# Kernel optimization log

Hardware: AMD Instinct MI355X
Metric: run time of the kernel (lower is better)

The kernel has to match this reference:

```python
import jax, jax.numpy as jnp
import numpy as np
from jax import lax

NEAR = 0.0
FAR = 2.4
NUM_STEPS = 16
NUM_REFINE = 8
LOG_THRESH = 0.0  # -log(1/0.5 - 1) for threshold=0.5
EPS = float(np.finfo(np.float32).eps)


def predict(points, feature, W1, b1, W2, b2, W3, b3):
    # points: [b, m, 3]; feature: [b, F] conditioning vector broadcast per point
    b, m, _ = points.shape
    feat = jnp.broadcast_to(feature[:, None, :], (b, m, feature.shape[-1]))
    x = jnp.concatenate([points, feat], axis=-1)
    h = jax.nn.relu(x @ W1 + b1)
    h = jax.nn.relu(h @ W2 + b2)
    return (h @ W3 + b3)[..., 0]  # [b, m] occupancy logits


def _safe_denom(dc):
    # torch.copysign(torch.max(torch.abs(dc), eps), dc)
    return jnp.copysign(jnp.maximum(jnp.abs(dc), EPS), dc)


def ray_march(ray0, ray_dirs, feature, params):
    b, n, _ = ray0.shape
    steps = jnp.linspace(0.0, 1.0, NUM_STEPS, dtype=ray0.dtype)
    dists = NEAR + steps * (FAR - NEAR)  # [S]
    # [b, n, S, 3]
    pts = ray0[:, :, None, :] + dists[None, None, :, None] * ray_dirs[:, :, None, :]
    f = predict(pts.reshape(b, n * NUM_STEPS, 3), feature, *params)
    f = f.reshape(b, n, NUM_STEPS) - LOG_THRESH
    # first outside->inside crossing per ray
    cross = (f[..., :-1] < 0) & (f[..., 1:] >= 0)  # [b, n, S-1]
    mask = jnp.any(cross, axis=-1)
    idx = jnp.argmax(cross, axis=-1)  # index of first crossing
    take = lambda a, i: jnp.take_along_axis(a, i[..., None], axis=-1)[..., 0]
    f_low = take(f, idx)
    f_high = take(f, idx + 1)
    d_low = dists[idx]
    d_high = dists[idx + 1]
    # secant refinement (fixed NUM_REFINE iterations, fully vectorized per ray)
    for _ in range(NUM_REFINE):
        d_new = d_low - f_low * (d_high - d_low) / _safe_denom(f_high - f_low)
        f_new = predict(ray0 + d_new[..., None] * ray_dirs, feature, *params) - LOG_THRESH
        below = f_new < 0
        d_low = jnp.where(below, d_new, d_low)
        f_low = jnp.where(below, f_new, f_low)
        d_high = jnp.where(below, d_high, d_new)
        f_high = jnp.where(below, f_new, f_high)
    d_pred = d_low - f_low * (d_high - d_low) / _safe_denom(f_high - f_low)
    d_pred = jnp.where(mask, d_pred, FAR)
    p_pred = ray0 + d_pred[..., None] * ray_dirs
    return d_pred, p_pred, mask


def setup_inputs() -> dict:
    key = jax.random.key(0)
    ks = jax.random.split(key, 6)
    B, N, F, H = 4, 16384, 32, 128
    ray0 = jax.random.normal(ks[0], (B, N, 3), jnp.float32) * 0.5
    rd = jax.random.normal(ks[1], (B, N, 3), jnp.float32)
    ray_dirs = rd / jnp.linalg.norm(rd, axis=-1, keepdims=True)
    feature = jax.random.normal(ks[2], (B, F), jnp.float32)
    W1 = jax.random.normal(ks[3], (3 + F, H), jnp.float32) / np.sqrt(3 + F)
    b1 = jnp.zeros((H,), jnp.float32)
    W2 = jax.random.normal(ks[4], (H, H), jnp.float32) / np.sqrt(H)
    b2 = jnp.zeros((H,), jnp.float32)
    W3 = jax.random.normal(ks[5], (H, 1), jnp.float32) / np.sqrt(H)
    b3 = jnp.zeros((1,), jnp.float32)
    return {"ray0": ray0, "ray_dirs": ray_dirs, "feature": feature,
            "W1": W1, "b1": b1, "W2": W2, "b2": b2, "W3": W3, "b3": b3}


def reference(ray0, ray_dirs, feature, W1, b1, W2, b2, W3, b3):
    params = (W1, b1, W2, b2, W3, b3)
    d_out, p_out, mask = ray_march(ray0, ray_dirs, feature, params)
    return d_out, p_out, mask
```

## Files before the change

### kernel.cpp

```cpp
#include <hip/hip_runtime.h>
#include <hip/hip_bf16.h>

typedef short short8 __attribute__((ext_vector_type(8)));
typedef float f32x4  __attribute__((ext_vector_type(4)));

static constexpr int   NPB  = 16384;
static constexpr int   NR   = 4 * NPB;
static constexpr int   NS   = 16;
static constexpr int   H    = 128;
static constexpr int   NPTS = NR * NS;
static constexpr int   NCHUNK2 = NR / 8;
static constexpr int   FIXCAP = 131072;
static constexpr float FARV = 2.4f;
static constexpr float EPSF = 1.1920928955078125e-07f;
static constexpr float FTHRESH = 0.03f;


__device__ __forceinline__ unsigned bf16hi(float x) {
    unsigned u = __float_as_uint(x);
    return (u + 0x7FFFu + ((u >> 16) & 1u)) >> 16;
}
__device__ __forceinline__ void split_bf16(float x, short& hi, short& lo) {
    unsigned h = bf16hi(x);
    float hf = __uint_as_float(h << 16);
    unsigned l = __float_as_uint(x - hf) >> 16;
    hi = (short)h; lo = (short)l;
}
__device__ __forceinline__ unsigned pk_bf16(float a, float b) {
    __hip_bfloat162 p = __float22bfloat162_rn(make_float2(a, b));
    unsigned u;
    __builtin_memcpy(&u, &p, sizeof(u));
    return u;
}

__global__ void k_setup(const float* __restrict__ W1, const float* __restrict__ b1,
                        const float* __restrict__ W2, const float* __restrict__ feat,
                        float* __restrict__ cva, short* __restrict__ w2f,
                        int* __restrict__ count, int* __restrict__ fixcnt)
{
    int t = blockIdx.x * blockDim.x + threadIdx.x;
    if (t == 0) { *count = 0; *fixcnt = 0; }
    if (t < 4 * H) {
        int b = t >> 7, kk = t & (H - 1);
        float acc = b1[kk];
#pragma unroll
        for (int i = 0; i < 32; ++i)
            acc = fmaf(feat[b * 32 + i], W1[(3 + i) * H + kk], acc);
        cva[b * H + kk] = acc;
    }
    {
        int lane = t & 63, ks = (t >> 6) & 3, part = (t >> 8) & 1;
        int nt = (t >> 9) & 1, w = (t >> 10) & 3;
        int n = w * 32 + nt * 16 + (lane & 15);
        int kb = ks * 32 + (lane >> 4) * 8;
        short8 v;
#pragma unroll
        for (int j = 0; j < 8; ++j) {
            short hi, lo;
            split_bf16(W2[(kb + j) * H + n], hi, lo);
            v[j] = part ? lo : hi;
        }
        ((short8*)w2f)[((w * 4 + nt * 2 + part) * 4 + ks) * 64 + lane] = v;
    }
}

__global__ __launch_bounds__(256, 2) void k_marchx(
    const float* __restrict__ ray0, const float* __restrict__ dirs,
    const float* __restrict__ W1,   const float* __restrict__ cva,
    const float* __restrict__ b2,   const float* __restrict__ W3,
    const float* __restrict__ b3p,  const short* __restrict__ w2f,
    float* __restrict__ f_all, int* __restrict__ fixlist, int* __restrict__ fixcnt)
{
    __shared__ __align__(16) short hAhi[16384];
    __shared__ float fpart[2][4][128];
    const int tid = threadIdx.x;
    const int w = tid >> 6, lane = tid & 63;
    const int q = lane >> 4, ln15 = lane & 15;

    const short8* wf8 = (const short8*)w2f;
    short8 Bh0[4], Bl0[4], Bh1[4], Bl1[4];
#pragma unroll
    for (int ks = 0; ks < 4; ++ks) {
        Bh0[ks] = wf8[((w * 4 + 0) * 4 + ks) * 64 + lane];
        Bl0[ks] = wf8[((w * 4 + 1) * 4 + ks) * 64 + lane];
        Bh1[ks] = wf8[((w * 4 + 2) * 4 + ks) * 64 + lane];
        Bl1[ks] = wf8[((w * 4 + 3) * 4 + ks) * 64 + lane];
    }
    const int nb0 = w * 32 + q * 4;
    float b2a[4], b2b[4], w3a[4], w3b[4];
#pragma unroll
    for (int reg = 0; reg < 4; ++reg) {
        b2a[reg] = b2[nb0 + reg];       b2b[reg] = b2[nb0 + 16 + reg];
        w3a[reg] = W3[nb0 + reg];       w3b[reg] = W3[nb0 + 16 + reg];
    }
    const float b3v  = *b3p;

    const int rr = tid & 7;
    const int kt = tid >> 3;
    const int qp = (tid >> 4) & 3;
    const int j0 = ((tid >> 3) & 1) * 4;
    short* hwp = hAhi + ((w * 64 + rr + 16 * qp) * 8 + j0);
    const float4 wxv = ((const float4*)W1)[kt];
    const float4 wyv = ((const float4*)(W1 + H))[kt];
    const float4 wzv = ((const float4*)(W1 + 2 * H))[kt];

    int pp = 0;
    for (int c = blockIdx.x; c < NCHUNK2; c += gridDim.x) {
        {
            int r = c * 8 + rr;
            float ox = ray0[3 * r], oy = ray0[3 * r + 1], oz = ray0[3 * r + 2];
            float dx = dirs[3 * r], dy = dirs[3 * r + 1], dz = dirs[3 * r + 2];
            const float4 cvv = ((const float4*)(cva + (r >> 14) * H))[kt];
            float bb0 = fmaf(ox, wxv.x, fmaf(oy, wyv.x, fmaf(oz, wzv.x, cvv.x)));
            float bb1 = fmaf(ox, wxv.y, fmaf(oy, wyv.y, fmaf(oz, wzv.y, cvv.y)));
            float bb2 = fmaf(ox, wxv.z, fmaf(oy, wyv.z, fmaf(oz, wzv.z, cvv.z)));
            float bb3 = fmaf(ox, wxv.w, fmaf(oy, wyv.w, fmaf(oz, wzv.w, cvv.w)));
            float sl0 = fmaf(dx, wxv.x, fmaf(dy, wyv.x, dz * wzv.x));
            float sl1 = fmaf(dx, wxv.y, fmaf(dy, wyv.y, dz * wzv.y));
            float sl2 = fmaf(dx, wxv.z, fmaf(dy, wyv.z, dz * wzv.z));
            float sl3 = fmaf(dx, wxv.w, fmaf(dy, wyv.w, dz * wzv.w));
#pragma unroll
            for (int s = 0; s < NS; ++s) {
                const float d = ((float)s * (1.0f / 15.0f)) * FARV;
                float h0 = fmaxf(fmaf(d, sl0, bb0), 0.0f);
                float h1 = fmaxf(fmaf(d, sl1, bb1), 0.0f);
                float h2 = fmaxf(fmaf(d, sl2, bb2), 0.0f);
                float h3 = fmaxf(fmaf(d, sl3, bb3), 0.0f);
                uint2 u;
                u.x = pk_bf16(h0, h1);
                u.y = pk_bf16(h2, h3);
                *(uint2*)(hwp + ((s >> 1) * 2048 + (s & 1) * 64)) = u;
            }
        }
        __syncthreads();
        const short8* hi8 = (const short8*)hAhi;
#pragma unroll 2
        for (int mt = 0; mt < 8; ++mt) {
            short8 Hh[4];
#pragma unroll
            for (int ks = 0; ks < 4; ++ks)
                Hh[ks] = hi8[(mt * 4 + ks) * 64 + lane];
            f32x4 a0 = {b2a[0], b2a[1], b2a[2], b2a[3]};
            f32x4 a1 = {b2b[0], b2b[1], b2b[2], b2b[3]};
#pragma unroll
            for (int ks = 0; ks < 4; ++ks) {
                a0 = __builtin_amdgcn_mfma_f32_16x16x32_bf16(Bh0[ks], Hh[ks], a0, 0, 0, 0);
                a1 = __builtin_amdgcn_mfma_f32_16x16x32_bf16(Bh1[ks], Hh[ks], a1, 0, 0, 0);
                a0 = __builtin_amdgcn_mfma_f32_16x16x32_bf16(Bl0[ks], Hh[ks], a0, 0, 0, 0);
                a1 = __builtin_amdgcn_mfma_f32_16x16x32_bf16(Bl1[ks], Hh[ks], a1, 0, 0, 0);
            }
            float fp0 = 0.0f, fp1 = 0.0f;
#pragma unroll
            for (int reg = 0; reg < 4; ++reg) {
                fp0 = fmaf(fmaxf(a0[reg], 0.f), w3a[reg], fp0);
                fp1 = fmaf(fmaxf(a1[reg], 0.f), w3b[reg], fp1);
            }
            float fp = fp0 + fp1;
            fp += __shfl_xor(fp, 16, 64);
            fp += __shfl_xor(fp, 32, 64);
            if (lane < 16) fpart[pp][w][mt * 16 + lane] = fp;
        }
        __syncthreads();
        if (tid < 128) {
            float f = fpart[pp][0][tid] + fpart[pp][1][tid] + fpart[pp][2][tid]
                    + fpart[pp][3][tid] + b3v;
            int s = tid >> 3, rb = tid & 7;
            int P = s * NR + c * 8 + rb;
            f_all[P] = f;
            if (fabsf(f) < FTHRESH) {
                int sl = atomicAdd(fixcnt, 1);
                if (sl < FIXCAP) fixlist[sl] = P;
            }
        }
        pp ^= 1;
    }
}

__global__ __launch_bounds__(256) void k_fix(
    const float* __restrict__ ray0, const float* __restrict__ dirs,
    const float* __restrict__ W1,   const float* __restrict__ cva,
    const float* __restrict__ W2,   const float* __restrict__ b2,
    const float* __restrict__ W3,   const float* __restrict__ b3p,
    const int* __restrict__ fixcnt, const int* __restrict__ fixlist,
    float* __restrict__ f_all)
{
    __shared__ __align__(16) float hsh[4][128][4];
    const int wv = threadIdx.x >> 6, lane = threadIdx.x & 63;
    unsigned fc = (unsigned)*fixcnt;
    if (fc > (unsigned)FIXCAP) fc = FIXCAP;

    const float w1x0 = W1[lane],           w1x1 = W1[64 + lane];
    const float w1y0 = W1[H + lane],       w1y1 = W1[H + 64 + lane];
    const float w1z0 = W1[2 * H + lane],   w1z1 = W1[2 * H + 64 + lane];
    const float w30  = W3[lane],           w31  = W3[64 + lane];
    const float b20  = b2[lane],           b21  = b2[64 + lane];
    const float b3v  = *b3p;

    for (unsigned i0 = (blockIdx.x * 4u + (unsigned)wv) * 4u; i0 < fc;
         i0 += gridDim.x * 16u) {
        int Pj[4];
#pragma unroll
        for (int j = 0; j < 4; ++j) {
            unsigned i = i0 + (unsigned)j;
            bool vld = (i < fc);
            int P = fixlist[vld ? i : i0] & (NPTS - 1);
            Pj[j] = vld ? P : -1;
            int r = P & (NR - 1), s = P >> 16;
            float d = ((float)s * (1.0f / 15.0f)) * FARV;
            float ox = ray0[3 * r], oy = ray0[3 * r + 1], oz = ray0[3 * r + 2];
            float dx = dirs[3 * r], dy = dirs[3 * r + 1], dz = dirs[3 * r + 2];
            float px = fmaf(d, dx, ox), py = fmaf(d, dy, oy), pz = fmaf(d, dz, oz);
            const float* __restrict__ cv = cva + (r >> 14) * H;
            float h0 = fmaf(px, w1x0, fmaf(py, w1y0, fmaf(pz, w1z0, cv[lane])));
            float h1 = fmaf(px, w1x1, fmaf(py, w1y1, fmaf(pz, w1z1, cv[64 + lane])));
            hsh[wv][lane][j]      = fmaxf(h0, 0.0f);
            hsh[wv][lane + 64][j] = fmaxf(h1, 0.0f);
        }
        float a0[4] = {b20, b20, b20, b20};
        float a1[4] = {b21, b21, b21, b21};
#pragma unroll 4
        for (int k = 0; k < H; ++k) {
            float4 hk = *(const float4*)&hsh[wv][k][0];
            float w2l = W2[k * H + lane];
            float w2h = W2[k * H + 64 + lane];
            a0[0] = fmaf(hk.x, w2l, a0[0]);  a1[0] = fmaf(hk.x, w2h, a1[0]);
            a0[1] = fmaf(hk.y, w2l, a0[1]);  a1[1] = fmaf(hk.y, w2h, a1[1]);
            a0[2] = fmaf(hk.z, w2l, a0[2]);  a1[2] = fmaf(hk.z, w2h, a1[2]);
            a0[3] = fmaf(hk.w, w2l, a0[3]);  a1[3] = fmaf(hk.w, w2h, a1[3]);
        }
#pragma unroll
        for (int j = 0; j < 4; ++j) {
            float f = fmaf(fmaxf(a0[j], 0.f), w30, fmaxf(a1[j], 0.f) * w31);
#pragma unroll
            for (int off = 32; off; off >>= 1)
                f += __shfl_xor(f, off, 64);
            if (lane == 0 && Pj[j] >= 0) f_all[Pj[j]] = f + b3v;
        }
    }
}

__global__ void k_cross(
    const float* __restrict__ ray0, const float* __restrict__ dirs,
    const float* __restrict__ f_all,
    int* __restrict__ count, int* __restrict__ ids,
    float4* __restrict__ state, float* __restrict__ out)
{
    int r = blockIdx.x * blockDim.x + threadIdx.x;
    float fv[NS];
#pragma unroll
    for (int s = 0; s < NS; ++s) fv[s] = f_all[s * NR + r];
    int idx = -1;
#pragma unroll
    for (int s = NS - 2; s >= 0; --s) {
        if (fv[s] < 0.0f && fv[s + 1] >= 0.0f) idx = s;
    }
    if (idx < 0) {
        float ox = ray0[3 * r], oy = ray0[3 * r + 1], oz = ray0[3 * r + 2];
        float dx = dirs[3 * r], dy = dirs[3 * r + 1], dz = dirs[3 * r + 2];
        out[r] = FARV;
        out[NR + 3 * r + 0] = fmaf(FARV, dx, ox);
        out[NR + 3 * r + 1] = fmaf(FARV, dy, oy);
        out[NR + 3 * r + 2] = fmaf(FARV, dz, oz);
        out[4 * NR + r] = 0.0f;
    } else {
        int slot = atomicAdd(count, 1);
        ids[slot] = r;
        float flo = fv[idx], fhi = fv[idx + 1];
        float dlo = ((float)idx * (1.0f / 15.0f)) * FARV;
        float dhi = ((float)(idx + 1) * (1.0f / 15.0f)) * FARV;
        state[slot] = make_float4(dlo, flo, dhi, fhi);
    }
}

__global__ __launch_bounds__(256, 2) void k_refine(
    const float* __restrict__ ray0, const float* __restrict__ dirs,
    const float* __restrict__ W1,   const float* __restrict__ cva,
    const float* __restrict__ b2,   const float* __restrict__ W3,
    const float* __restrict__ b3p,  const short* __restrict__ w2f,
    const int* __restrict__ count,  const int* __restrict__ ids,
    const float4* __restrict__ state, float* __restrict__ out)
{
    __shared__ __align__(16) short hAhi[2048];
    __shared__ __align__(16) short hAlo[2048];
    __shared__ float fpart[4][16];
    const int tid = threadIdx.x;
    const int w = tid >> 6, lane = tid & 63;
    const int q = lane >> 4, ln15 = lane & 15;

    unsigned cnt = (unsigned)*count;
    if (cnt > (unsigned)NR) cnt = (unsigned)NR;
    const unsigned g = blockIdx.x;
    if (g * 16u >= cnt) return;

    const short8* wf8 = (const short8*)w2f;
    short8 Bh0[4], Bl0[4], Bh1[4], Bl1[4];
#pragma unroll
    for (int ks = 0; ks < 4; ++ks) {
        Bh0[ks] = wf8[((w * 4 + 0) * 4 + ks) * 64 + lane];
        Bl0[ks] = wf8[((w * 4 + 1) * 4 + ks) * 64 + lane];
        Bh1[ks] = wf8[((w * 4 + 2) * 4 + ks) * 64 + lane];
        Bl1[ks] = wf8[((w * 4 + 3) * 4 + ks) * 64 + lane];
    }
    const int nb0 = w * 32 + q * 4;
    float b2a[4], b2b[4], w3a[4], w3b[4];
#pragma unroll
    for (int reg = 0; reg < 4; ++reg) {
        b2a[reg] = b2[nb0 + reg];       b2b[reg] = b2[nb0 + 16 + reg];
        w3a[reg] = W3[nb0 + reg];       w3b[reg] = W3[nb0 + 16 + reg];
    }
    const float b3v  = *b3p;

    const int i4 = (w * 32 + q * 8) >> 2;
    const float4* W1x4 = (const float4*)(W1);
    const float4* W1y4 = (const float4*)(W1 + H);
    const float4* W1z4 = (const float4*)(W1 + 2 * H);
    const float4 x0 = W1x4[i4], x1 = W1x4[i4 + 1];
    const float4 y0 = W1y4[i4], y1 = W1y4[i4 + 1];
    const float4 z0 = W1z4[i4], z1 = W1z4[i4 + 1];

    uint4* hi4 = (uint4*)hAhi;
    uint4* lo4 = (uint4*)hAlo;
    const short8* hi8 = (const short8*)hAhi;
    const short8* lo8 = (const short8*)hAlo;

    {
        unsigned t = g * 16u + (unsigned)ln15;
        bool valid = (t < cnt);
        unsigned tc = valid ? t : (cnt - 1);
        int r = ids[tc] & (NR - 1);
        float4 st = state[tc];
        float dlo = st.x, dhi = st.z;
        float flo = st.y, fhi = st.w;
        float ox = ray0[3 * r], oy = ray0[3 * r + 1], oz = ray0[3 * r + 2];
        float dx = dirs[3 * r], dy = dirs[3 * r + 1], dz = dirs[3 * r + 2];
        const float4* cv4 = (const float4*)(cva + (r >> 14) * H);
        float4 c0 = cv4[i4], c1 = cv4[i4 + 1];
        float dp = 0.0f;

#pragma unroll 1
        for (int it = 0; it < 9; ++it) {
            float dc  = fhi - flo;
            float den = copysignf(fmaxf(fabsf(dc), EPSF), dc);
            float dn  = dlo - (flo * (dhi - dlo)) / den;
            if (it == 8) { dp = dn; break; }
            float px = fmaf(dn, dx, ox), py = fmaf(dn, dy, oy), pz = fmaf(dn, dz, oz);
            float hv[8];
            hv[0] = fmaf(px, x0.x, fmaf(py, y0.x, fmaf(pz, z0.x, c0.x)));
            hv[1] = fmaf(px, x0.y, fmaf(py, y0.y, fmaf(pz, z0.y, c0.y)));
            hv[2] = fmaf(px, x0.z, fmaf(py, y0.z, fmaf(pz, z0.z, c0.z)));
            hv[3] = fmaf(px, x0.w, fmaf(py, y0.w, fmaf(pz, z0.w, c0.w)));
            hv[4] = fmaf(px, x1.x, fmaf(py, y1.x, fmaf(pz, z1.x, c1.x)));
            hv[5] = fmaf(px, x1.y, fmaf(py, y1.y, fmaf(pz, z1.y, c1.y)));
            hv[6] = fmaf(px, x1.z, fmaf(py, y1.z, fmaf(pz, z1.z, c1.z)));
            hv[7] = fmaf(px, x1.w, fmaf(py, y1.w, fmaf(pz, z1.w, c1.w)));
            unsigned uh[4], ul[4];
#pragma unroll
            for (int jp = 0; jp < 4; ++jp) {
                float h0 = fmaxf(hv[2 * jp],     0.0f);
                float h1 = fmaxf(hv[2 * jp + 1], 0.0f);
                unsigned u = pk_bf16(h0, h1);
                float hf0 = __uint_as_float(u << 16);
                float hf1 = __uint_as_float(u & 0xFFFF0000u);
                ul[jp] = pk_bf16(h0 - hf0, h1 - hf1);
                uh[jp] = u;
            }
            hi4[w * 64 + lane] = make_uint4(uh[0], uh[1], uh[2], uh[3]);
            lo4[w * 64 + lane] = make_uint4(ul[0], ul[1], ul[2], ul[3]);
            __syncthreads();
            short8 Ah[4], Al[4];
#pragma unroll
            for (int ks = 0; ks < 4; ++ks) {
                Ah[ks] = hi8[ks * 64 + lane];
                Al[ks] = lo8[ks * 64 + lane];
            }
            f32x4 hh0 = {b2a[0], b2a[1], b2a[2], b2a[3]};
            f32x4 hh1 = {b2b[0], b2b[1], b2b[2], b2b[3]};
            f32x4 lh0 = {0.f, 0.f, 0.f, 0.f}, lh1 = {0.f, 0.f, 0.f, 0.f};
            f32x4 hl0 = {0.f, 0.f, 0.f, 0.f}, hl1 = {0.f, 0.f, 0.f, 0.f};
#pragma unroll
            for (int ks = 0; ks < 4; ++ks) {
                hh0 = __builtin_amdgcn_mfma_f32_16x16x32_bf16(Bh0[ks], Ah[ks], hh0, 0, 0, 0);
                hh1 = __builtin_amdgcn_mfma_f32_16x16x32_bf16(Bh1[ks], Ah[ks], hh1, 0, 0, 0);
                lh0 = __builtin_amdgcn_mfma_f32_16x16x32_bf16(Bh0[ks], Al[ks], lh0, 0, 0, 0);
                lh1 = __builtin_amdgcn_mfma_f32_16x16x32_bf16(Bh1[ks], Al[ks], lh1, 0, 0, 0);
                hl0 = __builtin_amdgcn_mfma_f32_16x16x32_bf16(Bl0[ks], Ah[ks], hl0, 0, 0, 0);
                hl1 = __builtin_amdgcn_mfma_f32_16x16x32_bf16(Bl1[ks], Ah[ks], hl1, 0, 0, 0);
            }
            float fp = 0.0f;
#pragma unroll
            for (int reg = 0; reg < 4; ++reg) {
                float a0v = (hh0[reg] + lh0[reg]) + hl0[reg];
                float a1v = (hh1[reg] + lh1[reg]) + hl1[reg];
                fp = fmaf(fmaxf(a0v, 0.f), w3a[reg], fp);
                fp = fmaf(fmaxf(a1v, 0.f), w3b[reg], fp);
            }
            fp += __shfl_xor(fp, 16, 64);
            fp += __shfl_xor(fp, 32, 64);
            if (lane < 16) fpart[w][lane] = fp;
            __syncthreads();
            float fn = fpart[0][ln15] + fpart[1][ln15] + fpart[2][ln15]
                     + fpart[3][ln15] + b3v;
            bool bel = (fn < 0.0f);
            dlo = bel ? dn  : dlo;  flo = bel ? fn  : flo;
            dhi = bel ? dhi : dn;   fhi = bel ? fhi : fn;
        }
        if (tid < 16 && valid) {
            out[r] = dp;
            out[NR + 3 * r + 0] = fmaf(dp, dx, ox);
            out[NR + 3 * r + 1] = fmaf(dp, dy, oy);
            out[NR + 3 * r + 2] = fmaf(dp, dz, oz);
            out[4 * NR + r] = 1.0f;
        }
    }
}

extern "C" void kernel_launch(void* const* d_in, const int* in_sizes, int n_in,
                              void* d_out, int out_size, void* d_ws, size_t ws_size,
                              hipStream_t stream)
{
    const float* ray0 = (const float*)d_in[0];
    const float* dirs = (const float*)d_in[1];
    const float* feat = (const float*)d_in[2];
    const float* W1   = (const float*)d_in[3];
    const float* b1   = (const float*)d_in[4];
    const float* W2   = (const float*)d_in[5];
    const float* b2   = (const float*)d_in[6];
    const float* W3   = (const float*)d_in[7];
    const float* b3   = (const float*)d_in[8];
    float* out = (float*)d_out;

    float* w      = (float*)d_ws;
    short* w2f    = (short*)w;
    float* cva    = w + 16384;
    float* f_all  = w + 16896;
    float* stf    = w + 1065472;
    int*   ids    = (int*)(w + 1327616);
    int*   fixlist= (int*)(w + 1393152);
    int*   count  = (int*)(w + 1524224);
    int*   fixcnt = (int*)(w + 1524225);

    k_setup <<<16,   256, 0, stream>>>(W1, b1, W2, feat, cva, w2f, count, fixcnt);
    k_marchx<<<1024, 256, 0, stream>>>(ray0, dirs, W1, cva, b2, W3, b3, w2f,
                                       f_all, fixlist, fixcnt);
    k_fix   <<<1024, 256, 0, stream>>>(ray0, dirs, W1, cva, W2, b2, W3, b3,
                                       fixcnt, fixlist, f_all);
    k_cross <<<NR / 256, 256, 0, stream>>>(ray0, dirs, f_all, count, ids,
                                           (float4*)stf, out);
    k_refine<<<4096, 256, 0, stream>>>(ray0, dirs, W1, cva, b2, W3, b3, w2f,
                                       count, ids, (const float4*)stf, out);
}
```

Measured before the change: 181.3 us.

## Fuse crossing detection into refine kernel and widen march chunks to 16 rays

Removes the separate k_cross kernel. Each k_refine block now reads f_all for its 16 contiguous rays, finds the first crossing itself, and exits early when no ray in the wavefront crosses. This drops one launch plus the atomic compaction and the ids/state round-trip, but refine blocks no longer work on compacted rays, so blocks that mix crossing and non-crossing rays run MFMA work for idle lanes. Separately, k_marchx now processes 16 rays per chunk, with each thread computing 8 hidden units and writing uint4. This doubles shared memory to 64KB per block, which may lower occupancy.

```diff
diff --git a/kernel.cpp b/kernel.cpp
--- a/kernel.cpp
+++ b/kernel.cpp
@@ -9,7 +9,7 @@
 static constexpr int   NS   = 16;
 static constexpr int   H    = 128;
 static constexpr int   NPTS = NR * NS;
-static constexpr int   NCHUNK2 = NR / 8;
+static constexpr int   NCHUNKM = NR / 16;
 static constexpr int   FIXCAP = 131072;
 static constexpr float FARV = 2.4f;
 static constexpr float EPSF = 1.1920928955078125e-07f;
@@ -71,11 +71,11 @@
     const float* __restrict__ b3p,  const short* __restrict__ w2f,
     float* __restrict__ f_all, int* __restrict__ fixlist, int* __restrict__ fixcnt)
 {
-    __shared__ __align__(16) short hAhi[16384];
-    __shared__ float fpart[2][4][128];
+    __shared__ __align__(16) short hA[32768];
+    __shared__ float fpart[2][4][256];
     const int tid = threadIdx.x;
     const int w = tid >> 6, lane = tid & 63;
-    const int q = lane >> 4, ln15 = lane & 15;
+    const int q = lane >> 4;
 
     const short8* wf8 = (const short8*)w2f;
     short8 Bh0[4], Bl0[4], Bh1[4], Bl1[4];
@@ -95,30 +95,40 @@
     }
     const float b3v  = *b3p;
 
-    const int rr = tid & 7;
-    const int kt = tid >> 3;
-    const int qp = (tid >> 4) & 3;
-    const int j0 = ((tid >> 3) & 1) * 4;
-    short* hwp = hAhi + ((w * 64 + rr + 16 * qp) * 8 + j0);
-    const float4 wxv = ((const float4*)W1)[kt];
-    const float4 wyv = ((const float4*)(W1 + H))[kt];
-    const float4 wzv = ((const float4*)(W1 + 2 * H))[kt];
+    const int rr = tid & 15;
+    const int ko = tid >> 4;
+    short* hwp = hA + (((ko >> 2) * 64 + (ko & 3) * 16 + rr) * 8);
+    const float4* W1x4 = (const float4*)(W1);
+    const float4* W1y4 = (const float4*)(W1 + H);
+    const float4* W1z4 = (const float4*)(W1 + 2 * H);
 
     int pp = 0;
-    for (int c = blockIdx.x; c < NCHUNK2; c += gridDim.x) {
+    for (int c = blockIdx.x; c < NCHUNKM; c += gridDim.x) {
         {
-            int r = c * 8 + rr;
+            int r = c * 16 + rr;
             float ox = ray0[3 * r], oy = ray0[3 * r + 1], oz = ray0[3 * r + 2];
             float dx = dirs[3 * r], dy = dirs[3 * r + 1], dz = dirs[3 * r + 2];
-            const float4 cvv = ((const float4*)(cva + (r >> 14) * H))[kt];
-            float bb0 = fmaf(ox, wxv.x, fmaf(oy, wyv.x, fmaf(oz, wzv.x, cvv.x)));
-            float bb1 = fmaf(ox, wxv.y, fmaf(oy, wyv.y, fmaf(oz, wzv.y, cvv.y)));
-            float bb2 = fmaf(ox, wxv.z, fmaf(oy, wyv.z, fmaf(oz, wzv.z, cvv.z)));
-            float bb3 = fmaf(ox, wxv.w, fmaf(oy, wyv.w, fmaf(oz, wzv.w, cvv.w)));
-            float sl0 = fmaf(dx, wxv.x, fmaf(dy, wyv.x, dz * wzv.x));
-            float sl1 = fmaf(dx, wxv.y, fmaf(dy, wyv.y, dz * wzv.y));
-            float sl2 = fmaf(dx, wxv.z, fmaf(dy, wyv.z, dz * wzv.z));
-            float sl3 = fmaf(dx, wxv.w, fmaf(dy, wyv.w, dz * wzv.w));
+            const float4* cv4 = (const float4*)(cva + ((c * 16) >> 14) * H);
+            float4 x0 = W1x4[2 * ko], x1 = W1x4[2 * ko + 1];
+            float4 y0 = W1y4[2 * ko], y1 = W1y4[2 * ko + 1];
+            float4 z0 = W1z4[2 * ko], z1 = W1z4[2 * ko + 1];
+            float4 c0 = cv4[2 * ko],  c1 = cv4[2 * ko + 1];
+            float bb0 = fmaf(ox, x0.x, fmaf(oy, y0.x, fmaf(oz, z0.x, c0.x)));
+            float bb1 = fmaf(ox, x0.y, fmaf(oy, y0.y, fmaf(oz, z0.y, c0.y)));
+            float bb2 = fmaf(ox, x0.z, fmaf(oy, y0.z, fmaf(oz, z0.z, c0.z)));
+            float bb3 = fmaf(ox, x0.w, fmaf(oy, y0.w, fmaf(oz, z0.w, c0.w)));
+            float bb4 = fmaf(ox, x1.x, fmaf(oy, y1.x, fmaf(oz, z1.x, c1.x)));
+            float bb5 = fmaf(ox, x1.y, fmaf(oy, y1.y, fmaf(oz, z1.y, c1.y)));
+            float bb6 = fmaf(ox, x1.z, fmaf(oy, y1.z, fmaf(oz, z1.z, c1.z)));
+            float bb7 = fmaf(ox, x1.w, fmaf(oy, y1.w, fmaf(oz, z1.w, c1.w)));
+            float sl0 = fmaf(dx, x0.x, fmaf(dy, y0.x, dz * z0.x));
+            float sl1 = fmaf(dx, x0.y, fmaf(dy, y0.y, dz * z0.y));
+            float sl2 = fmaf(dx, x0.z, fmaf(dy, y0.z, dz * z0.z));
+            float sl3 = fmaf(dx, x0.w, fmaf(dy, y0.w, dz * z0.w));
+            float sl4 = fmaf(dx, x1.x, fmaf(dy, y1.x, dz * z1.x));
+            float sl5 = fmaf(dx, x1.y, fmaf(dy, y1.y, dz * z1.y));
+            float sl6 = fmaf(dx, x1.z, fmaf(dy, y1.z, dz * z1.z));
+            float sl7 = fmaf(dx, x1.w, fmaf(dy, y1.w, dz * z1.w));
 #pragma unroll
             for (int s = 0; s < NS; ++s) {
                 const float d = ((float)s * (1.0f / 15.0f)) * FARV;
@@ -126,16 +136,19 @@
                 float h1 = fmaxf(fmaf(d, sl1, bb1), 0.0f);
                 float h2 = fmaxf(fmaf(d, sl2, bb2), 0.0f);
                 float h3 = fmaxf(fmaf(d, sl3, bb3), 0.0f);
-                uint2 u;
-                u.x = pk_bf16(h0, h1);
-                u.y = pk_bf16(h2, h3);
-                *(uint2*)(hwp + ((s >> 1) * 2048 + (s & 1) * 64)) = u;
+                float h4 = fmaxf(fmaf(d, sl4, bb4), 0.0f);
+                float h5 = fmaxf(fmaf(d, sl5, bb5), 0.0f);
+                float h6 = fmaxf(fmaf(d, sl6, bb6), 0.0f);
+                float h7 = fmaxf(fmaf(d, sl7, bb7), 0.0f);
+                uint4 u = make_uint4(pk_bf16(h0, h1), pk_bf16(h2, h3),
+                                     pk_bf16(h4, h5), pk_bf16(h6, h7));
+                *(uint4*)(hwp + s * 2048) = u;
             }
         }
         __syncthreads();
-        const short8* hi8 = (const short8*)hAhi;
+        const short8* hi8 = (const short8*)hA;
 #pragma unroll 2
-        for (int mt = 0; mt < 8; ++mt) {
+        for (int mt = 0; mt < 16; ++mt) {
             short8 Hh[4];
 #pragma unroll
             for (int ks = 0; ks < 4; ++ks)
@@ -161,11 +174,11 @@
             if (lane < 16) fpart[pp][w][mt * 16 + lane] = fp;
         }
         __syncthreads();
-        if (tid < 128) {
+        {
             float f = fpart[pp][0][tid] + fpart[pp][1][tid] + fpart[pp][2][tid]
                     + fpart[pp][3][tid] + b3v;
-            int s = tid >> 3, rb = tid & 7;
-            int P = s * NR + c * 8 + rb;
+            int s = tid >> 4, rb = tid & 15;
+            int P = s * NR + c * 16 + rb;
             f_all[P] = f;
             if (fabsf(f) < FTHRESH) {
                 int sl = atomicAdd(fixcnt, 1);
@@ -239,46 +252,12 @@
     }
 }
 
-__global__ void k_cross(
-    const float* __restrict__ ray0, const float* __restrict__ dirs,
-    const float* __restrict__ f_all,
-    int* __restrict__ count, int* __restrict__ ids,
-    float4* __restrict__ state, float* __restrict__ out)
-{
-    int r = blockIdx.x * blockDim.x + threadIdx.x;
-    float fv[NS];
-#pragma unroll
-    for (int s = 0; s < NS; ++s) fv[s] = f_all[s * NR + r];
-    int idx = -1;
-#pragma unroll
-    for (int s = NS - 2; s >= 0; --s) {
-        if (fv[s] < 0.0f && fv[s + 1] >= 0.0f) idx = s;
-    }
-    if (idx < 0) {
-        float ox = ray0[3 * r], oy = ray0[3 * r + 1], oz = ray0[3 * r + 2];
-        float dx = dirs[3 * r], dy = dirs[3 * r + 1], dz = dirs[3 * r + 2];
-        out[r] = FARV;
-        out[NR + 3 * r + 0] = fmaf(FARV, dx, ox);
-        out[NR + 3 * r + 1] = fmaf(FARV, dy, oy);
-        out[NR + 3 * r + 2] = fmaf(FARV, dz, oz);
-        out[4 * NR + r] = 0.0f;
-    } else {
-        int slot = atomicAdd(count, 1);
-        ids[slot] = r;
-        float flo = fv[idx], fhi = fv[idx + 1];
-        float dlo = ((float)idx * (1.0f / 15.0f)) * FARV;
-        float dhi = ((float)(idx + 1) * (1.0f / 15.0f)) * FARV;
-        state[slot] = make_float4(dlo, flo, dhi, fhi);
-    }
-}
-
 __global__ __launch_bounds__(256, 2) void k_refine(
     const float* __restrict__ ray0, const float* __restrict__ dirs,
     const float* __restrict__ W1,   const float* __restrict__ cva,
     const float* __restrict__ b2,   const float* __restrict__ W3,
     const float* __restrict__ b3p,  const short* __restrict__ w2f,
-    const int* __restrict__ count,  const int* __restrict__ ids,
-    const float4* __restrict__ state, float* __restrict__ out)
+    const float* __restrict__ f_all, float* __restrict__ out)
 {
     __shared__ __align__(16) short hAhi[2048];
     __shared__ __align__(16) short hAlo[2048];
@@ -287,10 +266,35 @@
     const int w = tid >> 6, lane = tid & 63;
     const int q = lane >> 4, ln15 = lane & 15;
 
-    unsigned cnt = (unsigned)*count;
-    if (cnt > (unsigned)NR) cnt = (unsigned)NR;
-    const unsigned g = blockIdx.x;
-    if (g * 16u >= cnt) return;
+    const int rbase = blockIdx.x * 16;
+    const int r = rbase + ln15;
+
+    float fv[NS];
+#pragma unroll
+    for (int s = 0; s < NS; ++s) fv[s] = f_all[s * NR + r];
+    int idx = -1;
+#pragma unroll
+    for (int s = NS - 2; s >= 0; --s) {
+        if (fv[s] < 0.0f && fv[s + 1] >= 0.0f) idx = s;
+    }
+    const bool crossed = (idx >= 0);
+    float ox = ray0[3 * r], oy = ray0[3 * r + 1], oz = ray0[3 * r + 2];
+    float dx = dirs[3 * r], dy = dirs[3 * r + 1], dz = dirs[3 * r + 2];
+
+    if (!__any(crossed)) {
+        if (tid < 16) {
+            out[r] = FARV;
+            out[NR + 3 * r + 0] = fmaf(FARV, dx, ox);
+            out[NR + 3 * r + 1] = fmaf(FARV, dy, oy);
+            out[NR + 3 * r + 2] = fmaf(FARV, dz, oz);
+            out[4 * NR + r] = 0.0f;
+        }
+        return;
+    }
+    const int ic = crossed ? idx : 0;
+    float dlo = ((float)ic * (1.0f / 15.0f)) * FARV;
+    float dhi = ((float)(ic + 1) * (1.0f / 15.0f)) * FARV;
+    float flo = fv[ic], fhi = fv[ic + 1];
 
     const short8* wf8 = (const short8*)w2f;
     short8 Bh0[4], Bl0[4], Bh1[4], Bl1[4];
@@ -317,99 +321,95 @@
     const float4 x0 = W1x4[i4], x1 = W1x4[i4 + 1];
     const float4 y0 = W1y4[i4], y1 = W1y4[i4 + 1];
     const float4 z0 = W1z4[i4], z1 = W1z4[i4 + 1];
+    const float4* cv4 = (const float4*)(cva + (r >> 14) * H);
+    const float4 c0 = cv4[i4], c1 = cv4[i4 + 1];
 
     uint4* hi4 = (uint4*)hAhi;
     uint4* lo4 = (uint4*)hAlo;
     const short8* hi8 = (const short8*)hAhi;
     const short8* lo8 = (const short8*)hAlo;
 
-    {
-        unsigned t = g * 16u + (unsigned)ln15;
-        bool valid = (t < cnt);
-        unsigned tc = valid ? t : (cnt - 1);
-        int r = ids[tc] & (NR - 1);
-        float4 st = state[tc];
-        float dlo = st.x, dhi = st.z;
-        float flo = st.y, fhi = st.w;
-        float ox = ray0[3 * r], oy = ray0[3 * r + 1], oz = ray0[3 * r + 2];
-        float dx = dirs[3 * r], dy = dirs[3 * r + 1], dz = dirs[3 * r + 2];
-        const float4* cv4 = (const float4*)(cva + (r >> 14) * H);
-        float4 c0 = cv4[i4], c1 = cv4[i4 + 1];
-        float dp = 0.0f;
-
+    float dp = 0.0f;
 #pragma unroll 1
-        for (int it = 0; it < 9; ++it) {
-            float dc  = fhi - flo;
-            float den = copysignf(fmaxf(fabsf(dc), EPSF), dc);
-            float dn  = dlo - (flo * (dhi - dlo)) / den;
-            if (it == 8) { dp = dn; break; }
-            float px = fmaf(dn, dx, ox), py = fmaf(dn, dy, oy), pz = fmaf(dn, dz, oz);
-            float hv[8];
-            hv[0] = fmaf(px, x0.x, fmaf(py, y0.x, fmaf(pz, z0.x, c0.x)));
-            hv[1] = fmaf(px, x0.y, fmaf(py, y0.y, fmaf(pz, z0.y, c0.y)));
-            hv[2] = fmaf(px, x0.z, fmaf(py, y0.z, fmaf(pz, z0.z, c0.z)));
-            hv[3] = fmaf(px, x0.w, fmaf(py, y0.w, fmaf(pz, z0.w, c0.w)));
-            hv[4] = fmaf(px, x1.x, fmaf(py, y1.x, fmaf(pz, z1.x, c1.x)));
-            hv[5] = fmaf(px, x1.y, fmaf(py, y1.y, fmaf(pz, z1.y, c1.y)));
-            hv[6] = fmaf(px, x1.z, fmaf(py, y1.z, fmaf(pz, z1.z, c1.z)));
-            hv[7] = fmaf(px, x1.w, fmaf(py, y1.w, fmaf(pz, z1.w, c1.w)));
-            unsigned uh[4], ul[4];
-#pragma unroll
-            for (int jp = 0; jp < 4; ++jp) {
-                float h0 = fmaxf(hv[2 * jp],     0.0f);
-                float h1 = fmaxf(hv[2 * jp + 1], 0.0f);
-                unsigned u = pk_bf16(h0, h1);
-                float hf0 = __uint_as_float(u << 16);
-                float hf1 = __uint_as_float(u & 0xFFFF0000u);
-                ul[jp] = pk_bf16(h0 - hf0, h1 - hf1);
-                uh[jp] = u;
-            }
-            hi4[w * 64 + lane] = make_uint4(uh[0], uh[1], uh[2], uh[3]);
-            lo4[w * 64 + lane] = make_uint4(ul[0], ul[1], ul[2], ul[3]);
-            __syncthreads();
-            short8 Ah[4], Al[4];
-#pragma unroll
-            for (int ks = 0; ks < 4; ++ks) {
-                Ah[ks] = hi8[ks * 64 + lane];
-                Al[ks] = lo8[ks * 64 + lane];
-            }
-            f32x4 hh0 = {b2a[0], b2a[1], b2a[2], b2a[3]};
-            f32x4 hh1 = {b2b[0], b2b[1], b2b[2], b2b[3]};
-            f32x4 lh0 = {0.f, 0.f, 0.f, 0.f}, lh1 = {0.f, 0.f, 0.f, 0.f};
-            f32x4 hl0 = {0.f, 0.f, 0.f, 0.f}, hl1 = {0.f, 0.f, 0.f, 0.f};
-#pragma unroll
-            for (int ks = 0; ks < 4; ++ks) {
-                hh0 = __builtin_amdgcn_mfma_f32_16x16x32_bf16(Bh0[ks], Ah[ks], hh0, 0, 0, 0);
-                hh1 = __builtin_amdgcn_mfma_f32_16x16x32_bf16(Bh1[ks], Ah[ks], hh1, 0, 0, 0);
-                lh0 = __builtin_amdgcn_mfma_f32_16x16x32_bf16(Bh0[ks], Al[ks], lh0, 0, 0, 0);
-                lh1 = __builtin_amdgcn_mfma_f32_16x16x32_bf16(Bh1[ks], Al[ks], lh1, 0, 0, 0);
-                hl0 = __builtin_amdgcn_mfma_f32_16x16x32_bf16(Bl0[ks], Ah[ks], hl0, 0, 0, 0);
-                hl1 = __builtin_amdgcn_mfma_f32_16x16x32_bf16(Bl1[ks], Ah[ks], hl1, 0, 0, 0);
-            }
-            float fp = 0.0f;
-#pragma unroll
-            for (int reg = 0; reg < 4; ++reg) {
-                float a0v = (hh0[reg] + lh0[reg]) + hl0[reg];
-                float a1v = (hh1[reg] + lh1[reg]) + hl1[reg];
-                fp = fmaf(fmaxf(a0v, 0.f), w3a[reg], fp);
-                fp = fmaf(fmaxf(a1v, 0.f), w3b[reg], fp);
-            }
-            fp += __shfl_xor(fp, 16, 64);
-            fp += __shfl_xor(fp, 32, 64);
-            if (lane < 16) fpart[w][lane] = fp;
-            __syncthreads();
-            float fn = fpart[0][ln15] + fpart[1][ln15] + fpart[2][ln15]
-                     + fpart[3][ln15] + b3v;
-            bool bel = (fn < 0.0f);
-            dlo = bel ? dn  : dlo;  flo = bel ? fn  : flo;
-            dhi = bel ? dhi : dn;   fhi = bel ? fhi : fn;
-        }
-        if (tid < 16 && valid) {
+    for (int it = 0; it < 9; ++it) {
+        float dc  = fhi - flo;
+        float den = copysignf(fmaxf(fabsf(dc), EPSF), dc);
+        float dn  = dlo - (flo * (dhi - dlo)) / den;
+        if (it == 8) { dp = dn; break; }
+        float px = fmaf(dn, dx, ox), py = fmaf(dn, dy, oy), pz = fmaf(dn, dz, oz);
+        float hv[8];
+        hv[0] = fmaf(px, x0.x, fmaf(py, y0.x, fmaf(pz, z0.x, c0.x)));
+        hv[1] = fmaf(px, x0.y, fmaf(py, y0.y, fmaf(pz, z0.y, c0.y)));
+        hv[2] = fmaf(px, x0.z, fmaf(py, y0.z, fmaf(pz, z0.z, c0.z)));
+        hv[3] = fmaf(px, x0.w, fmaf(py, y0.w, fmaf(pz, z0.w, c0.w)));
+        hv[4] = fmaf(px, x1.x, fmaf(py, y1.x, fmaf(pz, z1.x, c1.x)));
+        hv[5] = fmaf(px, x1.y, fmaf(py, y1.y, fmaf(pz, z1.y, c1.y)));
+        hv[6] = fmaf(px, x1.z, fmaf(py, y1.z, fmaf(pz, z1.z, c1.z)));
+        hv[7] = fmaf(px, x1.w, fmaf(py, y1.w, fmaf(pz, z1.w, c1.w)));
+        unsigned uh[4], ul[4];
+#pragma unroll
+        for (int jp = 0; jp < 4; ++jp) {
+            float h0 = fmaxf(hv[2 * jp],     0.0f);
+            float h1 = fmaxf(hv[2 * jp + 1], 0.0f);
+            unsigned u = pk_bf16(h0, h1);
+            float hf0 = __uint_as_float(u << 16);
+            float hf1 = __uint_as_float(u & 0xFFFF0000u);
+            ul[jp] = pk_bf16(h0 - hf0, h1 - hf1);
+            uh[jp] = u;
+        }
+        hi4[w * 64 + lane] = make_uint4(uh[0], uh[1], uh[2], uh[3]);
+        lo4[w * 64 + lane] = make_uint4(ul[0], ul[1], ul[2], ul[3]);
+        __syncthreads();
+        short8 Ah[4], Al[4];
+#pragma unroll
+        for (int ks = 0; ks < 4; ++ks) {
+            Ah[ks] = hi8[ks * 64 + lane];
+            Al[ks] = lo8[ks * 64 + lane];
+        }
+        f32x4 hh0 = {b2a[0], b2a[1], b2a[2], b2a[3]};
+        f32x4 hh1 = {b2b[0], b2b[1], b2b[2], b2b[3]};
+        f32x4 lh0 = {0.f, 0.f, 0.f, 0.f}, lh1 = {0.f, 0.f, 0.f, 0.f};
+        f32x4 hl0 = {0.f, 0.f, 0.f, 0.f}, hl1 = {0.f, 0.f, 0.f, 0.f};
+#pragma unroll
+        for (int ks = 0; ks < 4; ++ks) {
+            hh0 = __builtin_amdgcn_mfma_f32_16x16x32_bf16(Bh0[ks], Ah[ks], hh0, 0, 0, 0);
+            hh1 = __builtin_amdgcn_mfma_f32_16x16x32_bf16(Bh1[ks], Ah[ks], hh1, 0, 0, 0);
+            lh0 = __builtin_amdgcn_mfma_f32_16x16x32_bf16(Bh0[ks], Al[ks], lh0, 0, 0, 0);
+            lh1 = __builtin_amdgcn_mfma_f32_16x16x32_bf16(Bh1[ks], Al[ks], lh1, 0, 0, 0);
+            hl0 = __builtin_amdgcn_mfma_f32_16x16x32_bf16(Bl0[ks], Ah[ks], hl0, 0, 0, 0);
+            hl1 = __builtin_amdgcn_mfma_f32_16x16x32_bf16(Bl1[ks], Ah[ks], hl1, 0, 0, 0);
+        }
+        float fp = 0.0f;
+#pragma unroll
+        for (int reg = 0; reg < 4; ++reg) {
+            float a0v = (hh0[reg] + lh0[reg]) + hl0[reg];
+            float a1v = (hh1[reg] + lh1[reg]) + hl1[reg];
+            fp = fmaf(fmaxf(a0v, 0.f), w3a[reg], fp);
+            fp = fmaf(fmaxf(a1v, 0.f), w3b[reg], fp);
+        }
+        fp += __shfl_xor(fp, 16, 64);
+        fp += __shfl_xor(fp, 32, 64);
+        if (lane < 16) fpart[w][lane] = fp;
+        __syncthreads();
+        float fn = fpart[0][ln15] + fpart[1][ln15] + fpart[2][ln15]
+                 + fpart[3][ln15] + b3v;
+        bool bel = (fn < 0.0f);
+        dlo = bel ? dn  : dlo;  flo = bel ? fn  : flo;
+        dhi = bel ? dhi : dn;   fhi = bel ? fhi : fn;
+    }
+    if (tid < 16) {
+        if (crossed) {
             out[r] = dp;
             out[NR + 3 * r + 0] = fmaf(dp, dx, ox);
             out[NR + 3 * r + 1] = fmaf(dp, dy, oy);
             out[NR + 3 * r + 2] = fmaf(dp, dz, oz);
             out[4 * NR + r] = 1.0f;
+        } else {
+            out[r] = FARV;
+            out[NR + 3 * r + 0] = fmaf(FARV, dx, ox);
+            out[NR + 3 * r + 1] = fmaf(FARV, dy, oy);
+            out[NR + 3 * r + 2] = fmaf(FARV, dz, oz);
+            out[4 * NR + r] = 0.0f;
         }
     }
 }
@@ -433,8 +433,6 @@
     short* w2f    = (short*)w;
     float* cva    = w + 16384;
     float* f_all  = w + 16896;
-    float* stf    = w + 1065472;
-    int*   ids    = (int*)(w + 1327616);
     int*   fixlist= (int*)(w + 1393152);
     int*   count  = (int*)(w + 1524224);
     int*   fixcnt = (int*)(w + 1524225);
@@ -444,8 +442,6 @@
                                        f_all, fixlist, fixcnt);
     k_fix   <<<1024, 256, 0, stream>>>(ray0, dirs, W1, cva, W2, b2, W3, b3,
                                        fixcnt, fixlist, f_all);
-    k_cross <<<NR / 256, 256, 0, stream>>>(ray0, dirs, f_all, count, ids,
-                                           (float4*)stf, out);
-    k_refine<<<4096, 256, 0, stream>>>(ray0, dirs, W1, cva, b2, W3, b3, w2f,
-                                       count, ids, (const float4*)stf, out);
-}
+    k_refine<<<NR / 16, 256, 0, stream>>>(ray0, dirs, W1, cva, b2, W3, b3, w2f,
+                                          f_all, out);
+}
```

After: 222.5 us. 22.7% more time.
